# Kernel tuning notes

Measured on AMD Instinct MI355X. Metric: run time of the kernel, lower is better.

Reference implementation:

```python
import jax, jax.numpy as jnp
import numpy as np


def setup_inputs() -> dict:
    key = jax.random.key(0)
    k0, k1, k2, k3, k4, k5 = jax.random.split(key, 6)
    B, H, P, L = 8, 128, 128, 4096
    u = jax.random.normal(k0, (B, H, L), dtype=jnp.float32)
    C2 = jax.random.normal(k1, (H, P, 2), dtype=jnp.float32)        # view_as_real(C)
    B_bar2 = jax.random.normal(k2, (P, H, 2), dtype=jnp.float32)    # view_as_real(B_bar)
    D = jax.random.normal(k3, (H, H), dtype=jnp.float32)
    # Frozen discrete diagonal state matrix: |lambda| in [strong, weak] = [0.9, 1.0]
    r = 0.9 + 0.1 * jax.random.uniform(k4, (P,), dtype=jnp.float32)
    th = 2.0 * jnp.pi * jax.random.uniform(k5, (P,), dtype=jnp.float32)
    Lambda_bar2 = jnp.stack([r * jnp.cos(th), r * jnp.sin(th)], axis=-1)
    return {"u": u, "C2": C2, "B_bar2": B_bar2, "D": D, "Lambda_bar2": Lambda_bar2}


def reference(u, C2, B_bar2, D, Lambda_bar2):
    L = u.shape[-1]
    Lam = Lambda_bar2[:, 0] + 1j * Lambda_bar2[:, 1]           # (P,)
    omega = 2.0 * jnp.pi * jnp.fft.rfftfreq(L).astype(jnp.float32)  # (Lf,)
    # Cauchy-like frequency kernel: 1 / (i*omega - Lambda)  -> (P, Lf)
    kernel = 1.0 / (1j * omega[None, :] - Lam[:, None])
    C = C2[..., 0] + 1j * C2[..., 1]                           # (H, P)
    B_bar = B_bar2[..., 0] + 1j * B_bar2[..., 1]               # (P, H)
    U_s = jnp.fft.rfftn(u)                                     # n-dim FFT (faithful to torch.fft.rfftn(u))
    C_kernel = jnp.einsum('hp,pl->hpl', C, kernel)             # (H, P, Lf)
    G = jnp.einsum('hpl,pq->hql', C_kernel, B_bar)             # (H, H, Lf)
    Y_s = jnp.einsum('hql,bql->bhl', G, U_s) + jnp.einsum('hq,bql->bhl', D.astype(U_s.dtype), U_s)
    y = jnp.fft.irfftn(Y_s)                                    # (B, H, L)
    return jax.nn.gelu(y, approximate=False)                   # torch nn.GELU default = exact erf
```

## Files before the change

kernel.cpp:

```cpp
#include <hip/hip_runtime.h>
#include <math.h>

#define PI_F 3.14159265358979323846f
#define NB 8
#define NH 128
#define NL 4096
#define LF 2049
#define WB 2064
#define NT 16512

typedef float2 cpx;
typedef __attribute__((ext_vector_type(8))) short bf8v;
typedef __attribute__((ext_vector_type(4))) float f4;

#define MFMA16(a, b, c) __builtin_amdgcn_mfma_f32_16x16x32_bf16(a, b, c, 0, 0, 0)

__device__ __forceinline__ float gelu_exact(float x) {
  return 0.5f * x * (1.0f + erff(x * 0.70710678118654752f));
}
__device__ __forceinline__ unsigned short f2bf(float f) {
  unsigned int x = __float_as_uint(f);
  return (unsigned short)((x + 0x7FFFu + ((x >> 16) & 1u)) >> 16);
}
__device__ __forceinline__ float bf2f(unsigned short h) {
  return __uint_as_float((unsigned int)h << 16);
}
__device__ __forceinline__ unsigned int packpair(float re, float im) {
  return (unsigned int)f2bf(re) | ((unsigned int)f2bf(im) << 16);
}
__device__ __forceinline__ cpx cadd(cpx a, cpx b) { return make_float2(a.x + b.x, a.y + b.y); }
__device__ __forceinline__ cpx csub(cpx a, cpx b) { return make_float2(a.x - b.x, a.y - b.y); }
__device__ __forceinline__ cpx cmul(cpx a, cpx b) {
  return make_float2(fmaf(a.x, b.x, -a.y * b.y), fmaf(a.x, b.y, a.y * b.x));
}
template <int SGN>
__device__ __forceinline__ cpx mulJ(cpx a) {
  return (SGN < 0) ? make_float2(a.y, -a.x) : make_float2(-a.y, a.x);
}

__device__ __forceinline__ void wrM(unsigned short* __restrict__ H,
                                    unsigned short* __restrict__ L,
                                    int m, int k, float v) {
  size_t a = (size_t)(k >> 5) * 8192 +
             (size_t)(m * 4 + (((k >> 3) & 3) ^ (m & 3))) * 8 + (k & 7);
  unsigned short h = f2bf(v);
  H[a] = h;
  L[a] = f2bf(v - bf2f(h));
}

__device__ __forceinline__ void gload16(const unsigned short* g, unsigned short* l) {
  __builtin_amdgcn_global_load_lds(
      (const __attribute__((address_space(1))) unsigned int*)g,
      (__attribute__((address_space(3))) unsigned int*)l, 16, 0, 0);
}

#define SW(k) ((k) ^ (((k) >> 4) & 31))

template <int SGN>
__device__ __forceinline__ void dft8(cpx a[8]) {
  cpx t0 = cadd(a[0], a[4]), u0 = csub(a[0], a[4]);
  cpx t1 = cadd(a[1], a[5]), u1 = csub(a[1], a[5]);
  cpx t2 = cadd(a[2], a[6]), u2 = csub(a[2], a[6]);
  cpx t3 = cadd(a[3], a[7]), u3 = csub(a[3], a[7]);
  cpx E0 = cadd(t0, t2), E2 = csub(t0, t2);
  cpx ju2 = mulJ<SGN>(u2);
  cpx E1 = cadd(u0, ju2), E3 = csub(u0, ju2);
  cpx O0 = cadd(t1, t3), O2 = csub(t1, t3);
  cpx ju3 = mulJ<SGN>(u3);
  cpx O1 = cadd(u1, ju3), O3 = csub(u1, ju3);
  const float r = 0.70710678118654752f;
  const float S = (float)SGN;
  cpx w1O1 = make_float2(r * (O1.x - S * O1.y), r * (O1.y + S * O1.x));
  cpx w3O3 = make_float2(r * (-O3.x - S * O3.y), r * (S * O3.x - O3.y));
  cpx jO2 = mulJ<SGN>(O2);
  a[0] = cadd(E0, O0);   a[4] = csub(E0, O0);
  a[1] = cadd(E1, w1O1); a[5] = csub(E1, w1O1);
  a[2] = cadd(E2, jO2);  a[6] = csub(E2, jO2);
  a[3] = cadd(E3, w3O3); a[7] = csub(E3, w3O3);
}

template <int SGN>
__device__ __forceinline__ void dft4(cpx b[4]) {
  cpx s0 = cadd(b[0], b[2]), d0 = csub(b[0], b[2]);
  cpx s1 = cadd(b[1], b[3]), d1 = csub(b[1], b[3]);
  cpx jd1 = mulJ<SGN>(d1);
  b[0] = cadd(s0, s1); b[2] = csub(s0, s1);
  b[1] = cadd(d0, jd1); b[3] = csub(d0, jd1);
}

__device__ __forceinline__ void twid8(cpx a[8], float ang) {
  float s, c; __sincosf(ang, &s, &c);
  cpx w1 = make_float2(c, s);
  cpx w2 = cmul(w1, w1), w3 = cmul(w2, w1), w4 = cmul(w2, w2);
  cpx w5 = cmul(w3, w2), w6 = cmul(w3, w3), w7 = cmul(w4, w3);
  a[1] = cmul(a[1], w1); a[2] = cmul(a[2], w2); a[3] = cmul(a[3], w3);
  a[4] = cmul(a[4], w4); a[5] = cmul(a[5], w5); a[6] = cmul(a[6], w6);
  a[7] = cmul(a[7], w7);
}

template <int SGN>
__device__ __forceinline__ void fft2048_core(cpx a[8], cpx* __restrict__ bufA,
                                             cpx* __restrict__ bufB, int t) {
  const float S = (float)SGN;
  dft8<SGN>(a);
  twid8(a, S * (2.f * PI_F / 2048.f) * (float)t);
#pragma unroll
  for (int p = 0; p < 8; ++p) bufA[p * 264 + t] = a[p];
  __syncthreads();
  int p = t >> 5, n1 = t & 31;
#pragma unroll
  for (int j = 0; j < 8; ++j) a[j] = bufA[p * 264 + n1 + 32 * j];
  dft8<SGN>(a);
  twid8(a, S * (2.f * PI_F / 256.f) * (float)n1);
#pragma unroll
  for (int q = 0; q < 8; ++q) bufB[p * 264 + q * 33 + n1] = a[q];
  __syncthreads();
  int q = (t >> 2) & 7, n2 = t & 3;
#pragma unroll
  for (int j = 0; j < 8; ++j) a[j] = bufB[p * 264 + q * 33 + n2 + 4 * j];
  dft8<SGN>(a);
  twid8(a, S * (2.f * PI_F / 32.f) * (float)n2);
#pragma unroll
  for (int d = 0; d < 8; ++d) bufA[p * 264 + q * 33 + 4 * d + n2] = a[d];
  __syncthreads();
#pragma unroll
  for (int h = 0; h < 2; ++h) {
    int d = 2 * n2 + h;
    cpx b[4];
#pragma unroll
    for (int m = 0; m < 4; ++m) b[m] = bufA[p * 264 + q * 33 + 4 * d + m];
    dft4<SGN>(b);
    int kb = p + 8 * q + 64 * d;
#pragma unroll
    for (int c = 0; c < 4; ++c) bufB[SW(kb + 512 * c)] = b[c];
  }
  __syncthreads();
}

__global__ __launch_bounds__(256) void fwd_pre(
    const float* __restrict__ u,
    const float* __restrict__ C2, const float* __restrict__ B2,
    const float* __restrict__ D,
    unsigned int* __restrict__ Uph,
    unsigned short* __restrict__ Mbh, unsigned short* __restrict__ Mbl,
    unsigned short* __restrict__ Mch, unsigned short* __restrict__ Mcl) {
  __shared__ cpx bufA[2112], bufB[2112];
  int t = threadIdx.x;
  if (blockIdx.x < 192) {
    __shared__ float rc[128], rs[128];
    __shared__ float sTr[2][128], sTi[2][128];
    int e = blockIdx.x;
    int which = e >> 6;
    int half = t >> 7, tt = t & 127;
    int x = (2 * e + half) & 127;
    { float s, c; sincosf(-(2.f * PI_F / 128.f) * (float)tt, &s, &c); rc[tt] = c; rs[tt] = s; }
    __syncthreads();
    float sr = 0.f, si = 0.f;
    if (which == 0) {
      for (int k = 0; k < 128; ++k) {
        int j = (k * tt) & 127; float c = rc[j], s = rs[j];
        float br = B2[(x * 128 + k) * 2], bi = B2[(x * 128 + k) * 2 + 1];
        sr += br * c - bi * s; si += br * s + bi * c;
      }
      wrM(Mbh, Mbl, 2 * x,     2 * tt,     sr);
      wrM(Mbh, Mbl, 2 * x,     2 * tt + 1, -si);
      wrM(Mbh, Mbl, 2 * x + 1, 2 * tt,     si);
      wrM(Mbh, Mbl, 2 * x + 1, 2 * tt + 1,  sr);
    } else if (which == 1) {
      for (int k = 0; k < 128; ++k) {
        int j = (k * tt) & 127; float c = rc[j], s = -rs[j];
        float cr = C2[(k * 128 + x) * 2], ci = C2[(k * 128 + x) * 2 + 1];
        sr += cr * c - ci * s; si += cr * s + ci * c;
      }
      sr *= (1.f / 128.f); si *= (1.f / 128.f);
      wrM(Mch, Mcl, 2 * tt,     2 * x,     sr);
      wrM(Mch, Mcl, 2 * tt,     2 * x + 1, -si);
      wrM(Mch, Mcl, 2 * tt + 1, 2 * x,     si);
      wrM(Mch, Mcl, 2 * tt + 1, 2 * x + 1,  sr);
    } else {
      for (int k = 0; k < 128; ++k) {
        int j = (k * x) & 127; float c = rc[j], s = rs[j];
        float d = D[tt * 128 + k];
        sr += d * c; si += d * s;
      }
      sTr[half][tt] = sr; sTi[half][tt] = si;
      __syncthreads();
      sr = 0.f; si = 0.f;
      for (int k = 0; k < 128; ++k) {
        int j = (k * tt) & 127; float c = rc[j], s = -rs[j];
        sr += sTr[half][k] * c - sTi[half][k] * s;
        si += sTr[half][k] * s + sTi[half][k] * c;
      }
      sr *= (1.f / 128.f); si *= (1.f / 128.f);
      wrM(Mch, Mcl, 2 * tt,     256 + 2 * x,     sr);
      wrM(Mch, Mcl, 2 * tt,     256 + 2 * x + 1, -si);
      wrM(Mch, Mcl, 2 * tt + 1, 256 + 2 * x,     si);
      wrM(Mch, Mcl, 2 * tt + 1, 256 + 2 * x + 1,  sr);
    }
    return;
  }
  int row = blockIdx.x - 192;
  int b = row >> 7, q = row & 127;
  const cpx* src = (const cpx*)(u + (size_t)row * NL);
  cpx a[8];
#pragma unroll
  for (int j = 0; j < 8; ++j) a[j] = src[t + 256 * j];
  fft2048_core<-1>(a, bufA, bufB, t);
  unsigned int* Uh = Uph + (size_t)q * NT + (size_t)b * WB;
  auto pstore = [&](int k, float ur, float ui) { Uh[k] = packpair(ur, ui); };
#pragma unroll
  for (int r = 0; r < 4; ++r) {
    int k = t + (r << 8);
    if (k == 0) {
      cpx z0 = bufB[SW(0)];
      pstore(0, z0.x + z0.y, 0.f);
      pstore(2048, z0.x - z0.y, 0.f);
      cpx zN = bufB[SW(1024)];
      pstore(1024, zN.x, -zN.y);
    } else {
      cpx A = bufB[SW(k)];
      cpx M = bufB[SW(2048 - k)];
      float Br = M.x, Bi = -M.y;
      float sr = 0.5f * (A.x + Br), si = 0.5f * (A.y + Bi);
      float dr = 0.5f * (A.x - Br), di = 0.5f * (A.y - Bi);
      float th = (float)k * (PI_F / 2048.f);
      float sn, cs; __sincosf(th, &sn, &cs);
      float tr = cs * dr + sn * di;
      float ti = cs * di - sn * dr;
      pstore(k, sr + ti, si - tr);
      float A2r = M.x, A2i = M.y;
      float B2r = A.x, B2i = -A.y;
      float s2r = 0.5f * (A2r + B2r), s2i = 0.5f * (A2i + B2i);
      float d2r = 0.5f * (A2r - B2r), d2i = 0.5f * (A2i - B2i);
      float t2r = -cs * d2r + sn * d2i;
      float t2i = -cs * d2i - sn * d2r;
      pstore(2048 - k, s2r + t2i, s2i - t2r);
    }
  }
}

__global__ __launch_bounds__(256, 1) void gemm_fused(
    const unsigned short* __restrict__ Mbh, const unsigned short* __restrict__ Mbl,
    const unsigned short* __restrict__ Mch, const unsigned short* __restrict__ Mcl,
    const unsigned int* __restrict__ Uph,
    const float* __restrict__ Lam,
    float2* __restrict__ Yp) {
  __shared__ unsigned short Ah[2][8192], Al[2][8192];
  __shared__ unsigned int Vl[8448];
  int tid = threadIdx.x;
  int j0 = blockIdx.x * 64;
  int w = tid >> 6, lane = tid & 63, quad = lane >> 4, ln = lane & 15;

  unsigned int breg[2][4][4];
  f4 acc[4][4];

#define STAGE_A(H, L, tile, buf)                                              \
  {                                                                           \
    size_t tb_ = (size_t)(tile) * 8192;                                       \
    _Pragma("unroll") for (int r_ = 0; r_ < 4; ++r_) {                        \
      int sb_ = w * 256 + r_ * 64;                                            \
      gload16((H) + tb_ + (size_t)(sb_ + lane) * 8, &Ah[buf][sb_ * 8]);       \
      gload16((L) + tb_ + (size_t)(sb_ + lane) * 8, &Al[buf][sb_ * 8]);       \
    }                                                                         \
  }
#define LOAD_B(g, it)                                                         \
  {                                                                           \
    _Pragma("unroll") for (int nt_ = 0; nt_ < 4; ++nt_)                       \
      _Pragma("unroll") for (int c_ = 0; c_ < 4; ++c_)                        \
        breg[g][nt_][c_] =                                                    \
            Uph[(size_t)((it) * 16 + quad * 4 + c_) * NT + j0 + nt_ * 16 + ln]; \
  }
#define VMW(n) asm volatile("s_waitcnt vmcnt(" #n ")" ::: "memory")
#define LGW()  asm volatile("s_waitcnt lgkmcnt(0)" ::: "memory")

  auto bFromReg = [&](int g, bf8v bh[4]) {
#pragma unroll
    for (int nt = 0; nt < 4; ++nt) {
      union { unsigned int u[4]; bf8v v; } cv;
#pragma unroll
      for (int c = 0; c < 4; ++c) cv.u[c] = breg[g][nt][c];
      bh[nt] = cv.v;
    }
  };
  auto bFromV = [&](int i, bf8v bh[4]) {
    const unsigned short* Vs = (const unsigned short*)Vl;
#pragma unroll
    for (int nt = 0; nt < 4; ++nt)
      bh[nt] = *(const bf8v*)&Vs[(size_t)(i * 4 + quad) * 528 + (nt * 16 + ln) * 8];
  };
  auto compute = [&](int buf, const bf8v* bh) {
    bf8v ah[4], al[4];
#pragma unroll
    for (int mt = 0; mt < 4; ++mt) {
      int m = w * 64 + mt * 16 + ln;
      int off = (m * 4 + (quad ^ (m & 3))) * 8;
      ah[mt] = *(const bf8v*)&Ah[buf][off];
      al[mt] = *(const bf8v*)&Al[buf][off];
    }
#pragma unroll
    for (int mt = 0; mt < 4; ++mt)
#pragma unroll
      for (int nt = 0; nt < 4; ++nt) {
        acc[mt][nt] = MFMA16(ah[mt], bh[nt], acc[mt][nt]);
        acc[mt][nt] = MFMA16(al[mt], bh[nt], acc[mt][nt]);
      }
  };

  STAGE_A(Mbh, Mbl, 0, 0);
  LOAD_B(0, 0);
#pragma unroll
  for (int mt = 0; mt < 4; ++mt)
#pragma unroll
    for (int nt = 0; nt < 4; ++nt) acc[mt][nt] = (f4){0.f, 0.f, 0.f, 0.f};

#pragma unroll
  for (int i = 0; i < 8; ++i) {
    LGW();
    if (i < 7) {
      STAGE_A(Mbh, Mbl, i + 1, (i + 1) & 1);
      LOAD_B((i + 1) & 1, i + 1);
      VMW(24);
    } else {
      VMW(0);
    }
    bf8v bh[4];
    bFromReg(i & 1, bh);
    compute(i & 1, bh);
  }

#pragma unroll
  for (int mt = 0; mt < 4; ++mt) {
    int r0 = w * 64 + mt * 16 + quad * 4;
    int p0 = r0 >> 1;
    float2 lam0 = ((const float2*)Lam)[p0];
    float2 lam1 = ((const float2*)Lam)[p0 + 1];
#pragma unroll
    for (int nt = 0; nt < 4; ++nt) {
      int col = nt * 16 + ln;
      int gcol = j0 + col;
      int bb = gcol / WB; int l = gcol - bb * WB;
      float omega = (float)l * (PI_F / 2048.f);
      f4 a = acc[mt][nt];
      float dx0 = -lam0.x, dy0 = omega - lam0.y;
      float inv0 = 1.f / (dx0 * dx0 + dy0 * dy0);
      float kr0 = dx0 * inv0, ki0 = -dy0 * inv0;
      float v0r = kr0 * a[0] - ki0 * a[1];
      float v0i = kr0 * a[1] + ki0 * a[0];
      float dx1 = -lam1.x, dy1 = omega - lam1.y;
      float inv1 = 1.f / (dx1 * dx1 + dy1 * dy1);
      float kr1 = dx1 * inv1, ki1 = -dy1 * inv1;
      float v1r = kr1 * a[2] - ki1 * a[3];
      float v1i = kr1 * a[3] + ki1 * a[2];
      int ch = p0 >> 2;
      Vl[ch * 264 + col * 4 + (p0 & 3)] = packpair(v0r, v0i);
      Vl[ch * 264 + col * 4 + ((p0 + 1) & 3)] = packpair(v1r, v1i);
    }
  }
  __syncthreads();

  STAGE_A(Mch, Mcl, 0, 0);
#pragma unroll
  for (int mt = 0; mt < 4; ++mt)
#pragma unroll
    for (int nt = 0; nt < 4; ++nt) acc[mt][nt] = (f4){0.f, 0.f, 0.f, 0.f};

#pragma unroll
  for (int i = 0; i < 8; ++i) {
    LGW();
    if (i < 7) {
      STAGE_A(Mch, Mcl, i + 1, (i + 1) & 1);
      VMW(8);
    } else {
      STAGE_A(Mch, Mcl, 8, 0);
      LOAD_B(0, 0);
      VMW(24);
    }
    bf8v bh[4];
    bFromV(i, bh);
    compute(i & 1, bh);
  }
#pragma unroll
  for (int i = 8; i < 16; ++i) {
    LGW();
    if (i < 15) {
      STAGE_A(Mch, Mcl, i + 1, (i + 1) & 1);
      LOAD_B((i + 1) & 1, i + 1 - 8);
      VMW(24);
    } else {
      VMW(0);
    }
    bf8v bh[4];
    bFromReg(i & 1, bh);
    compute(i & 1, bh);
  }

#pragma unroll
  for (int mt = 0; mt < 4; ++mt) {
    int r0 = w * 64 + mt * 16 + quad * 4;
    int h0 = r0 >> 1;
#pragma unroll
    for (int nt = 0; nt < 4; ++nt) {
      int gcol = j0 + nt * 16 + ln;
      f4 a = acc[mt][nt];
      Yp[(size_t)h0 * NT + gcol] = make_float2(a[0], a[1]);
      Yp[(size_t)(h0 + 1) * NT + gcol] = make_float2(a[2], a[3]);
    }
  }
#undef STAGE_A
#undef LOAD_B
#undef VMW
#undef LGW
}

__global__ __launch_bounds__(256) void fft_inv_gelu_pl(const float2* __restrict__ Yp,
                                                       float* __restrict__ out) {
  __shared__ cpx bufA[2112], bufB[2112];
  int t = threadIdx.x;
  int row = blockIdx.x;
  int b = row >> 7, h = row & 127;
  const float2* Yrow = Yp + (size_t)h * NT + (size_t)b * WB;
#pragma unroll
  for (int r = 0; r < 4; ++r) {
    int k = t + (r << 8);
    if (k == 0) {
      float y0 = Yrow[0].x;
      float yN = Yrow[2048].x;
      bufB[SW(0)] = make_float2(0.5f * (y0 + yN), 0.5f * (y0 - yN));
      float2 z = Yrow[1024];
      bufB[SW(1024)] = make_float2(z.x, -z.y);
    } else {
      float2 A = Yrow[k];
      float2 M = Yrow[2048 - k];
      float Br = M.x, Bi = -M.y;
      float sr = 0.5f * (A.x + Br), si = 0.5f * (A.y + Bi);
      float dr = 0.5f * (A.x - Br), di = 0.5f * (A.y - Bi);
      float th = (float)k * (PI_F / 2048.f);
      float sn, cs; __sincosf(th, &sn, &cs);
      float e1 = cs * di + sn * dr;
      float e2 = cs * dr - sn * di;
      bufB[SW(k)] = make_float2(sr - e1, si + e2);
      bufB[SW(2048 - k)] = make_float2(sr + e1, -si + e2);
    }
  }
  __syncthreads();
  cpx a[8];
#pragma unroll
  for (int j = 0; j < 8; ++j) a[j] = bufB[SW(t + 256 * j)];
  fft2048_core<1>(a, bufA, bufB, t);
  float2* dst = (float2*)(out + (size_t)row * NL);
  const float sc = 1.f / 2048.f;
#pragma unroll
  for (int r = 0; r < 8; ++r) {
    int n = t + (r << 8);
    cpx z = bufB[SW(n)];
    dst[n] = make_float2(gelu_exact(z.x * sc), gelu_exact(z.y * sc));
  }
}

__global__ __launch_bounds__(128) void fb_precomp(
    const float* __restrict__ C2, const float* __restrict__ B2,
    const float* __restrict__ D,
    float* __restrict__ Bt, float* __restrict__ Ct, float* __restrict__ Dt) {
  __shared__ float rc[128], rs[128];
  __shared__ float sTr[128], sTi[128];
  int x = blockIdx.x, t = threadIdx.x, which = blockIdx.y;
  { float s, c; sincosf(-(2.f * PI_F / 128.f) * (float)t, &s, &c); rc[t] = c; rs[t] = s; }
  __syncthreads();
  float sr = 0.f, si = 0.f;
  if (which == 0) {
    for (int k = 0; k < 128; ++k) {
      int j = (k * t) & 127; float c = rc[j], s = rs[j];
      float br = B2[(x * 128 + k) * 2], bi = B2[(x * 128 + k) * 2 + 1];
      sr += br * c - bi * s; si += br * s + bi * c;
    }
    Bt[(t * 128 + x) * 2] = sr; Bt[(t * 128 + x) * 2 + 1] = si;
  } else if (which == 1) {
    for (int k = 0; k < 128; ++k) {
      int j = (k * t) & 127; float c = rc[j], s = -rs[j];
      float cr = C2[(k * 128 + x) * 2], ci = C2[(k * 128 + x) * 2 + 1];
      sr += cr * c - ci * s; si += cr * s + ci * c;
    }
    Ct[(x * 128 + t) * 2] = sr * (1.f / 128.f);
    Ct[(x * 128 + t) * 2 + 1] = si * (1.f / 128.f);
  } else {
    for (int k = 0; k < 128; ++k) {
      int j = (k * x) & 127; float c = rc[j], s = rs[j];
      float d = D[t * 128 + k];
      sr += d * c; si += d * s;
    }
    sTr[t] = sr; sTi[t] = si;
    __syncthreads();
    sr = 0.f; si = 0.f;
    for (int k = 0; k < 128; ++k) {
      int j = (k * t) & 127; float c = rc[j], s = -rs[j];
      sr += sTr[k] * c - sTi[k] * s;
      si += sTr[k] * s + sTi[k] * c;
    }
    Dt[(x * 128 + t) * 2] = sr * (1.f / 128.f);
    Dt[(x * 128 + t) * 2 + 1] = si * (1.f / 128.f);
  }
}

__global__ __launch_bounds__(256) void fb_fft_fwd(const float* __restrict__ u,
                                                  cpx* __restrict__ U) {
  __shared__ cpx bufA[2112], bufB[2112];
  int t = threadIdx.x;
  int row = blockIdx.x;
  const cpx* src = (const cpx*)(u + (size_t)row * NL);
  cpx a[8];
#pragma unroll
  for (int j = 0; j < 8; ++j) a[j] = src[t + 256 * j];
  fft2048_core<-1>(a, bufA, bufB, t);
  cpx* Urow = U + (size_t)row * LF;
#pragma unroll
  for (int r = 0; r < 4; ++r) {
    int k = t + (r << 8);
    if (k == 0) {
      cpx z0 = bufB[SW(0)];
      Urow[0] = make_float2(z0.x + z0.y, 0.f);
      Urow[2048] = make_float2(z0.x - z0.y, 0.f);
      cpx zN = bufB[SW(1024)];
      Urow[1024] = make_float2(zN.x, -zN.y);
    } else {
      cpx A = bufB[SW(k)];
      cpx M = bufB[SW(2048 - k)];
      float Br = M.x, Bi = -M.y;
      float sr = 0.5f * (A.x + Br), si = 0.5f * (A.y + Bi);
      float dr = 0.5f * (A.x - Br), di = 0.5f * (A.y - Bi);
      float th = (float)k * (PI_F / 2048.f);
      float sn, cs; __sincosf(th, &sn, &cs);
      float tr = cs * dr + sn * di;
      float ti = cs * di - sn * dr;
      Urow[k] = make_float2(sr + ti, si - tr);
      float A2r = M.x, A2i = M.y;
      float B2r = A.x, B2i = -A.y;
      float s2r = 0.5f * (A2r + B2r), s2i = 0.5f * (A2i + B2i);
      float d2r = 0.5f * (A2r - B2r), d2i = 0.5f * (A2i - B2i);
      float t2r = -cs * d2r + sn * d2i;
      float t2i = -cs * d2i - sn * d2r;
      Urow[2048 - k] = make_float2(s2r + t2i, s2i - t2r);
    }
  }
}

__device__ __forceinline__ void ld4(float4 d[4], const float4* __restrict__ p) {
#pragma unroll
  for (int kk = 0; kk < 4; ++kk) d[kk] = p[kk];
}
__device__ __forceinline__ void cmac4(const float4 m[4], float xr, float xi,
                                      float ar[8], float ai[8]) {
#pragma unroll
  for (int kk = 0; kk < 4; ++kk) {
    float4 v = m[kk];
    ar[2 * kk]     = fmaf(v.x, xr, fmaf(-v.y, xi, ar[2 * kk]));
    ai[2 * kk]     = fmaf(v.x, xi, fmaf( v.y, xr, ai[2 * kk]));
    ar[2 * kk + 1] = fmaf(v.z, xr, fmaf(-v.w, xi, ar[2 * kk + 1]));
    ai[2 * kk + 1] = fmaf(v.z, xi, fmaf( v.w, xr, ai[2 * kk + 1]));
  }
}

__global__ __launch_bounds__(256) void fb_mix(
    const cpx* __restrict__ U,
    const float* __restrict__ Bt, const float* __restrict__ Ct,
    const float* __restrict__ Dt, const float* __restrict__ Lam,
    cpx* __restrict__ Y) {
  __shared__ cpx sU[128][17], sV[128][17];
  int tid = threadIdx.x;
  int b = blockIdx.y;
  size_t ub = (size_t)b * NH * LF;
  if (blockIdx.x == 128) {
    int t = tid;
    if (t < 128) sU[t][0] = U[ub + (size_t)t * LF + 2048];
    __syncthreads();
    if (t < 128) {
      float ar = 0.f, ai = 0.f;
      for (int q = 0; q < 128; ++q) {
        float ur = sU[q][0].x, ui = sU[q][0].y;
        float br = Bt[(q * 128 + t) * 2], bi = Bt[(q * 128 + t) * 2 + 1];
        ar = fmaf(br, ur, fmaf(-bi, ui, ar));
        ai = fmaf(br, ui, fmaf(bi, ur, ai));
      }
      float a = Lam[2 * t], bb = Lam[2 * t + 1];
      float dx = -a, dy = PI_F - bb;
      float inv = 1.f / (dx * dx + dy * dy);
      float kr = dx * inv, ki = -dy * inv;
      sV[t][0] = make_float2(kr * ar - ki * ai, kr * ai + ki * ar);
    }
    __syncthreads();
    if (t < 128) {
      float ar = 0.f, ai = 0.f;
      for (int q = 0; q < 128; ++q) {
        float ur = sU[q][0].x, ui = sU[q][0].y;
        float vr = sV[q][0].x, vi = sV[q][0].y;
        float cr = Ct[(q * 128 + t) * 2], ci = Ct[(q * 128 + t) * 2 + 1];
        float dr = Dt[(q * 128 + t) * 2], di = Dt[(q * 128 + t) * 2 + 1];
        ar += cr * vr - ci * vi + dr * ur - di * ui;
        ai += cr * vi + ci * vr + dr * ui + di * ur;
      }
      Y[ub + (size_t)t * LF + 2048] = make_float2(ar, ai);
    }
    return;
  }
  int lane = tid & 15, g = tid >> 4;
  int l = blockIdx.x * 16 + lane;
#pragma unroll
  for (int rep = 0; rep < 8; ++rep) {
    int q = rep * 16 + g;
    sU[q][lane] = U[ub + (size_t)q * LF + l];
  }
  __syncthreads();
  float omega = (float)l * (PI_F / 2048.f);
  float ar[8], ai[8];
  {
#pragma unroll
    for (int k = 0; k < 8; ++k) { ar[k] = 0.f; ai[k] = 0.f; }
    const float4* base = (const float4*)Bt + g * 4;
    float4 e[4], o[4];
    ld4(e, base);
#pragma unroll 1
    for (int q = 0; q < 128; q += 2) {
      ld4(o, base + (q + 1) * 64);
      cpx u0 = sU[q][lane];
      cmac4(e, u0.x, u0.y, ar, ai);
      ld4(e, base + ((q + 2) & 127) * 64);
      cpx u1 = sU[q + 1][lane];
      cmac4(o, u1.x, u1.y, ar, ai);
    }
    int p0 = g * 8;
#pragma unroll
    for (int k = 0; k < 8; ++k) {
      int p = p0 + k;
      float a = Lam[2 * p], bb = Lam[2 * p + 1];
      float dx = -a, dy = omega - bb;
      float inv = 1.f / (dx * dx + dy * dy);
      float kr = dx * inv, ki = -dy * inv;
      sV[p][lane] = make_float2(kr * ar[k] - ki * ai[k], kr * ai[k] + ki * ar[k]);
    }
  }
  __syncthreads();
  {
#pragma unroll
    for (int k = 0; k < 8; ++k) { ar[k] = 0.f; ai[k] = 0.f; }
    const float4* base = (const float4*)Ct + g * 4;
    float4 e[4], o[4];
    ld4(e, base);
#pragma unroll 1
    for (int q = 0; q < 128; q += 2) {
      ld4(o, base + (q + 1) * 64);
      cpx v0 = sV[q][lane];
      cmac4(e, v0.x, v0.y, ar, ai);
      ld4(e, base + ((q + 2) & 127) * 64);
      cpx v1 = sV[q + 1][lane];
      cmac4(o, v1.x, v1.y, ar, ai);
    }
  }
  {
    const float4* base = (const float4*)Dt + g * 4;
    float4 e[4], o[4];
    ld4(e, base);
#pragma unroll 1
    for (int q = 0; q < 128; q += 2) {
      ld4(o, base + (q + 1) * 64);
      cpx u0 = sU[q][lane];
      cmac4(e, u0.x, u0.y, ar, ai);
      ld4(e, base + ((q + 2) & 127) * 64);
      cpx u1 = sU[q + 1][lane];
      cmac4(o, u1.x, u1.y, ar, ai);
    }
  }
  int h0 = g * 8;
#pragma unroll
  for (int k = 0; k < 8; ++k) {
    Y[ub + (size_t)(h0 + k) * LF + l] = make_float2(ar[k], ai[k]);
  }
}

__global__ __launch_bounds__(256) void fb_fft_inv(const cpx* __restrict__ Y,
                                                  float* __restrict__ out) {
  __shared__ cpx bufA[2112], bufB[2112];
  int t = threadIdx.x;
  int row = blockIdx.x;
  const cpx* Yrow = Y + (size_t)row * LF;
#pragma unroll
  for (int r = 0; r < 4; ++r) {
    int k = t + (r << 8);
    if (k == 0) {
      float y0 = Yrow[0].x;
      float yN = Yrow[2048].x;
      bufB[SW(0)] = make_float2(0.5f * (y0 + yN), 0.5f * (y0 - yN));
      cpx z = Yrow[1024];
      bufB[SW(1024)] = make_float2(z.x, -z.y);
    } else {
      cpx A = Yrow[k];
      cpx M = Yrow[2048 - k];
      float Br = M.x, Bi = -M.y;
      float sr = 0.5f * (A.x + Br), si = 0.5f * (A.y + Bi);
      float dr = 0.5f * (A.x - Br), di = 0.5f * (A.y - Bi);
      float th = (float)k * (PI_F / 2048.f);
      float sn, cs; __sincosf(th, &sn, &cs);
      float e1 = cs * di + sn * dr;
      float e2 = cs * dr - sn * di;
      bufB[SW(k)] = make_float2(sr - e1, si + e2);
      bufB[SW(2048 - k)] = make_float2(sr + e1, -si + e2);
    }
  }
  __syncthreads();
  cpx a[8];
#pragma unroll
  for (int j = 0; j < 8; ++j) a[j] = bufB[SW(t + 256 * j)];
  fft2048_core<1>(a, bufA, bufB, t);
  float2* dst = (float2*)(out + (size_t)row * NL);
  const float sc = 1.f / 2048.f;
#pragma unroll
  for (int r = 0; r < 8; ++r) {
    int n = t + (r << 8);
    cpx z = bufB[SW(n)];
    dst[n] = make_float2(gelu_exact(z.x * sc), gelu_exact(z.y * sc));
  }
}

extern "C" void kernel_launch(void* const* d_in, const int* in_sizes, int n_in,
                              void* d_out, int out_size, void* d_ws, size_t ws_size,
                              hipStream_t stream) {
  const float* u   = (const float*)d_in[0];
  const float* C2  = (const float*)d_in[1];
  const float* B2  = (const float*)d_in[2];
  const float* D   = (const float*)d_in[3];
  const float* Lam = (const float*)d_in[4];
  float* out = (float*)d_out;

  const size_t PL = (size_t)128 * NT;
  const size_t need = PL * 4
                    + PL * 8
                    + 2 * 65536 * 2 + 2 * 131072 * 2;

  if (ws_size >= need) {
    unsigned int* Uph = (unsigned int*)d_ws;
    float2* Yp = (float2*)(Uph + PL);
    unsigned short* Mbh = (unsigned short*)(Yp + PL);
    unsigned short* Mbl = Mbh + 65536;
    unsigned short* Mch = Mbl + 65536;
    unsigned short* Mcl = Mch + 131072;

    fwd_pre<<<192 + NB * NH, 256, 0, stream>>>(u, C2, B2, D, Uph, Mbh, Mbl, Mch, Mcl);
    gemm_fused<<<NT / 64, 256, 0, stream>>>(Mbh, Mbl, Mch, Mcl, Uph, Lam, Yp);
    fft_inv_gelu_pl<<<NB * NH, 256, 0, stream>>>(Yp, out);
  } else {
    float* ws = (float*)d_ws;
    const size_t nUc = (size_t)NB * NH * LF;
    cpx* U  = (cpx*)ws;
    cpx* Yf = U;
    float* Bt = ws + 2 * nUc;
    float* Ct = Bt + 32768;
    float* Dt = Ct + 32768;
    fb_precomp<<<dim3(128, 3), 128, 0, stream>>>(C2, B2, D, Bt, Ct, Dt);
    fb_fft_fwd<<<NB * NH, 256, 0, stream>>>(u, U);
    fb_mix<<<dim3(129, NB), 256, 0, stream>>>(U, Bt, Ct, Dt, Lam, Yf);
    fb_fft_inv<<<NB * NH, 256, 0, stream>>>(Yf, out);
  }
}
```

Baseline: 139.7 us.

## Deepen B-operand register prefetch to three stages and overlap phase transition loads

In the fused GEMM kernel, the global-to-register prefetch of U spectrum tiles goes from double to triple buffering, so loads are issued two iterations ahead. The A-tile load for the second GEMM now starts during the tail of the first GEMM, and the full __syncthreads before it becomes a wait plus a raw barrier. The intent is to hide global memory latency across the two chained GEMMs, at the cost of more registers with launch bounds of one block per CU. Separately, the DFT precompute blocks stage B2/C2 rows in shared memory instead of doing strided global reads, and their inner loops are unrolled.

```diff
diff --git a/kernel.cpp b/kernel.cpp
--- a/kernel.cpp
+++ b/kernel.cpp
@@ -148,18 +148,27 @@
   int t = threadIdx.x;
   if (blockIdx.x < 192) {
     __shared__ float rc[128], rs[128];
+    __shared__ float sOr[2][128], sOi[2][128];
     __shared__ float sTr[2][128], sTi[2][128];
     int e = blockIdx.x;
     int which = e >> 6;
     int half = t >> 7, tt = t & 127;
     int x = (2 * e + half) & 127;
     { float s, c; sincosf(-(2.f * PI_F / 128.f) * (float)tt, &s, &c); rc[tt] = c; rs[tt] = s; }
+    if (which == 0) {
+      float2 v = ((const float2*)B2)[(size_t)x * 128 + tt];
+      sOr[half][tt] = v.x; sOi[half][tt] = v.y;
+    } else if (which == 1) {
+      float2 v = ((const float2*)C2)[(size_t)tt * 128 + x];
+      sOr[half][tt] = v.x; sOi[half][tt] = v.y;
+    }
     __syncthreads();
     float sr = 0.f, si = 0.f;
     if (which == 0) {
+#pragma unroll 4
       for (int k = 0; k < 128; ++k) {
         int j = (k * tt) & 127; float c = rc[j], s = rs[j];
-        float br = B2[(x * 128 + k) * 2], bi = B2[(x * 128 + k) * 2 + 1];
+        float br = sOr[half][k], bi = sOi[half][k];
         sr += br * c - bi * s; si += br * s + bi * c;
       }
       wrM(Mbh, Mbl, 2 * x,     2 * tt,     sr);
@@ -167,9 +176,10 @@
       wrM(Mbh, Mbl, 2 * x + 1, 2 * tt,     si);
       wrM(Mbh, Mbl, 2 * x + 1, 2 * tt + 1,  sr);
     } else if (which == 1) {
+#pragma unroll 4
       for (int k = 0; k < 128; ++k) {
         int j = (k * tt) & 127; float c = rc[j], s = -rs[j];
-        float cr = C2[(k * 128 + x) * 2], ci = C2[(k * 128 + x) * 2 + 1];
+        float cr = sOr[half][k], ci = sOi[half][k];
         sr += cr * c - ci * s; si += cr * s + ci * c;
       }
       sr *= (1.f / 128.f); si *= (1.f / 128.f);
@@ -178,6 +188,7 @@
       wrM(Mch, Mcl, 2 * tt + 1, 2 * x,     si);
       wrM(Mch, Mcl, 2 * tt + 1, 2 * x + 1,  sr);
     } else {
+#pragma unroll 8
       for (int k = 0; k < 128; ++k) {
         int j = (k * x) & 127; float c = rc[j], s = rs[j];
         float d = D[tt * 128 + k];
@@ -186,6 +197,7 @@
       sTr[half][tt] = sr; sTi[half][tt] = si;
       __syncthreads();
       sr = 0.f; si = 0.f;
+#pragma unroll 4
       for (int k = 0; k < 128; ++k) {
         int j = (k * tt) & 127; float c = rc[j], s = -rs[j];
         sr += sTr[half][k] * c - sTi[half][k] * s;
@@ -251,7 +263,7 @@
   int j0 = blockIdx.x * 64;
   int w = tid >> 6, lane = tid & 63, quad = lane >> 4, ln = lane & 15;
 
-  unsigned int breg[2][4][4];
+  unsigned int breg[3][4][4];
   f4 acc[4][4];
 
 #define STAGE_A(H, L, tile, buf)                                              \
@@ -308,24 +320,27 @@
 
   STAGE_A(Mbh, Mbl, 0, 0);
   LOAD_B(0, 0);
+  LOAD_B(1, 1);
 #pragma unroll
   for (int mt = 0; mt < 4; ++mt)
 #pragma unroll
     for (int nt = 0; nt < 4; ++nt) acc[mt][nt] = (f4){0.f, 0.f, 0.f, 0.f};
 
 #pragma unroll
-  for (int i = 0; i < 8; ++i) {
+  for (int i = 0; i < 6; ++i) {
     LGW();
-    if (i < 7) {
-      STAGE_A(Mbh, Mbl, i + 1, (i + 1) & 1);
-      LOAD_B((i + 1) & 1, i + 1);
-      VMW(24);
-    } else {
-      VMW(0);
-    }
-    bf8v bh[4];
-    bFromReg(i & 1, bh);
-    compute(i & 1, bh);
+    STAGE_A(Mbh, Mbl, i + 1, (i + 1) & 1);
+    LOAD_B((i + 2) % 3, i + 2);
+    VMW(40);
+    bf8v bh[4]; bFromReg(i % 3, bh); compute(i & 1, bh);
+  }
+  {
+    LGW(); STAGE_A(Mbh, Mbl, 7, 1); VMW(24);
+    bf8v bh[4]; bFromReg(0, bh); compute(0, bh);
+  }
+  {
+    LGW(); STAGE_A(Mch, Mcl, 0, 0); VMW(8);
+    bf8v bh[4]; bFromReg(1, bh); compute(1, bh);
   }
 
 #pragma unroll
@@ -356,42 +371,44 @@
       Vl[ch * 264 + col * 4 + ((p0 + 1) & 3)] = packpair(v1r, v1i);
     }
   }
-  __syncthreads();
-
-  STAGE_A(Mch, Mcl, 0, 0);
+  LGW();
+  __builtin_amdgcn_s_barrier();
+
 #pragma unroll
   for (int mt = 0; mt < 4; ++mt)
 #pragma unroll
     for (int nt = 0; nt < 4; ++nt) acc[mt][nt] = (f4){0.f, 0.f, 0.f, 0.f};
 
 #pragma unroll
-  for (int i = 0; i < 8; ++i) {
+  for (int i = 0; i < 6; ++i) {
     LGW();
-    if (i < 7) {
-      STAGE_A(Mch, Mcl, i + 1, (i + 1) & 1);
-      VMW(8);
-    } else {
-      STAGE_A(Mch, Mcl, 8, 0);
-      LOAD_B(0, 0);
-      VMW(24);
-    }
-    bf8v bh[4];
-    bFromV(i, bh);
-    compute(i & 1, bh);
-  }
-#pragma unroll
-  for (int i = 8; i < 16; ++i) {
+    STAGE_A(Mch, Mcl, i + 1, (i + 1) & 1);
+    VMW(8);
+    bf8v bh[4]; bFromV(i, bh); compute(i & 1, bh);
+  }
+  {
+    LGW(); STAGE_A(Mch, Mcl, 7, 1); LOAD_B(2, 0); VMW(24);
+    bf8v bh[4]; bFromV(6, bh); compute(0, bh);
+  }
+  {
+    LGW(); STAGE_A(Mch, Mcl, 8, 0); LOAD_B(0, 1); VMW(40);
+    bf8v bh[4]; bFromV(7, bh); compute(1, bh);
+  }
+#pragma unroll
+  for (int i = 8; i < 14; ++i) {
     LGW();
-    if (i < 15) {
-      STAGE_A(Mch, Mcl, i + 1, (i + 1) & 1);
-      LOAD_B((i + 1) & 1, i + 1 - 8);
-      VMW(24);
-    } else {
-      VMW(0);
-    }
-    bf8v bh[4];
-    bFromReg(i & 1, bh);
-    compute(i & 1, bh);
+    STAGE_A(Mch, Mcl, i + 1, (i + 1) & 1);
+    LOAD_B((i + 2) % 3, i + 2 - 8);
+    VMW(40);
+    bf8v bh[4]; bFromReg(i % 3, bh); compute(i & 1, bh);
+  }
+  {
+    LGW(); STAGE_A(Mch, Mcl, 15, 1); VMW(24);
+    bf8v bh[4]; bFromReg(2, bh); compute(0, bh);
+  }
+  {
+    LGW(); VMW(0);
+    bf8v bh[4]; bFromReg(0, bh); compute(1, bh);
   }
 
 #pragma unroll
```

Result: no change. 140.3 us (+0.4%).
